# Kernel optimization log

Measured on AMD Instinct MI355X. Metric: run time of the kernel, lower is better.

Reference implementation:

```python
import jax, jax.numpy as jnp
import numpy as np

PHI = 0.1  # fraction of pruned weights randomized per inference


def setup_inputs() -> dict:
    key = jax.random.key(0)
    k1, k2, k3 = jax.random.split(key, 3)
    d_out, d_in, batch = 8192, 8192, 256
    W = jax.random.normal(k1, (d_out, d_in), jnp.float32) * 0.02
    prune = jax.random.uniform(k2, (d_out, d_in)) < 0.9
    W = jnp.where(prune, 0.0, W)
    mask = (W == 0.0)  # _register_masks: pruned positions
    x = jax.random.normal(k3, (batch, d_in), jnp.float32)
    return {"x": x, "W": W, "mask": mask}


def reference(x, W, mask):
    # --- _apply_random_flip (vectorized) ---
    n_pruned = int(np.asarray(jnp.sum(mask)))          # concrete mask -> static count
    n_flip = max(1, int(PHI * n_pruned))
    keep = ~mask
    n_keep = jnp.sum(keep).astype(W.dtype)
    wk = jnp.where(keep, W, 0.0)
    mean = jnp.sum(wk) / n_keep
    # torch .std() is unbiased (n-1 denominator)
    var = jnp.sum(jnp.where(keep, (W - mean) ** 2, 0.0)) / (n_keep - 1.0)
    std = jnp.sqrt(var)
    key = jax.random.key(42)
    ks, kv = jax.random.split(key)
    # uniform random permutation of pruned indices -> top_k of random scores
    scores = jnp.where(mask.ravel(), jax.random.uniform(ks, (W.size,)), -1.0)
    _, flip_idx = jax.lax.top_k(scores, n_flip)        # [n_flip] flat indices into W
    vals = jax.random.normal(kv, (n_flip,), W.dtype) * std * 0.1
    W_flipped = W.ravel().at[flip_idx].set(vals).reshape(W.shape)
    # --- base_model forward (Linear, no bias) ---
    out = x @ W_flipped.T                               # [batch, d_out]
    # --- _restore_masks: zero flipped weights again (no effect on out) ---
    _ = jnp.where(mask, 0.0, W_flipped)
    return out
```

## Files before the change

kernel.cpp:

```cpp
#include <hip/hip_runtime.h>

typedef unsigned int u32;
typedef unsigned long long u64;
typedef unsigned short u16;

#define NTOT   67108864u
#define T0P    7543296u
#define PBASE  14733u
#define NSUP   1651u
#define NWSEG  4096u
#define WCAP   2176u
#define RBLK   512u
#define SEGPB  8
#define RCAP   4352u
#define KSPLIT 4

struct Scalars {
  double sumW;
  double sumW2;
  u64 npruned;
  u64 nflip;
  float stdf;
  float pad;
};

#define OFF_COLSUM 0ull
#define OFF_SBASE  8192ull
#define OFF_SC     16384ull
#define OFF_SEGCNT 16512ull
#define OFF_XBF    33024ull
#define OFF_SEGS   4227328ull
#define OFF_ROUTED 39878912ull
#define OFF_WBF    75530496ull
#define WS_NEED_WBF 209748224ull
#define OFF_OUTP   OFF_SEGS

__host__ __device__ inline void tf2x32(u32 k0, u32 k1, u32 x0, u32 x1, u32& y0, u32& y1) {
  u32 ks2 = k0 ^ k1 ^ 0x1BD11BDAu;
  x0 += k0; x1 += k1;
#define TFR(r) { x0 += x1; x1 = (x1 << (r)) | (x1 >> (32 - (r))); x1 ^= x0; }
  TFR(13) TFR(15) TFR(26) TFR(6)  x0 += k1;  x1 += ks2 + 1u;
  TFR(17) TFR(29) TFR(16) TFR(24) x0 += ks2; x1 += k0 + 2u;
  TFR(13) TFR(15) TFR(26) TFR(6)  x0 += k0;  x1 += k1 + 3u;
  TFR(17) TFR(29) TFR(16) TFR(24) x0 += k1;  x1 += ks2 + 4u;
  TFR(13) TFR(15) TFR(26) TFR(6)  x0 += ks2; x1 += k0 + 5u;
#undef TFR
  y0 = x0; y1 = x1;
}

__device__ inline u32 jax_bits32(u32 k0, u32 k1, u32 i) {
  u32 y0, y1; tf2x32(k0, k1, 0u, i, y0, y1);
  return y0 ^ y1;
}

__device__ inline u16 f2bf(float f) {
  union { float f; u32 u; } c; c.f = f;
  u32 r = ((c.u >> 16) & 1u) + 0x7FFFu;
  return (u16)((c.u + r) >> 16);
}

__device__ inline float erfinv32(float x) {
  float w = -log1pf(-x * x);
  float p;
  if (w < 5.0f) {
    w -= 2.5f;
    p = 2.81022636e-08f;
    p = fmaf(p, w, 3.43273939e-07f);
    p = fmaf(p, w, -3.5233877e-06f);
    p = fmaf(p, w, -4.39150654e-06f);
    p = fmaf(p, w, 0.00021858087f);
    p = fmaf(p, w, -0.00125372503f);
    p = fmaf(p, w, -0.00417768164f);
    p = fmaf(p, w, 0.246640727f);
    p = fmaf(p, w, 1.50140941f);
  } else {
    w = sqrtf(w) - 3.0f;
    p = -0.000200214257f;
    p = fmaf(p, w, 0.000100950558f);
    p = fmaf(p, w, 0.00134934322f);
    p = fmaf(p, w, -0.00367342844f);
    p = fmaf(p, w, 0.00573950773f);
    p = fmaf(p, w, -0.0076224613f);
    p = fmaf(p, w, 0.00943887047f);
    p = fmaf(p, w, 1.00167406f);
    p = fmaf(p, w, 2.83297682f);
  }
  return p * x;
}

__global__ __launch_bounds__(256) void k_pass1w(const float* __restrict__ W,
                                                u16* __restrict__ wbf,
                                                const float* __restrict__ x,
                                                u16* __restrict__ xbf,
                                                Scalars* sc, u32* segcnt, u32* segs,
                                                u32 uk0, u32 uk1, u32 dowbf) {
  u32 t = threadIdx.x;
  u32 bid = blockIdx.x;
  if (bid < 1024u) {
    u32 gid = bid * 256 + t;
    u32 lane = t & 63;
    u32 wid = gid >> 6;
    u32* wseg = segs + (u64)wid * WCAP;
    u32 wbase = 0;
    float sf = 0.f, sf2 = 0.f; u32 cnt = 0;
    const u32 stride8 = 1024u * 256u * 8u;
    for (u32 b8 = gid * 8; b8 < NTOT; b8 += stride8) {
      float4 wa = *(const float4*)(W + b8);
      float4 wb = *(const float4*)(W + b8 + 4);
      u32 sb[8];
#pragma unroll
      for (int e = 0; e < 8; e++) sb[e] = jax_bits32(uk0, uk1, b8 + (u32)e) >> 9;
      float we[8] = {wa.x, wa.y, wa.z, wa.w, wb.x, wb.y, wb.z, wb.w};
      u32 cand[8]; u32 nc = 0;
#pragma unroll
      for (int e = 0; e < 8; e++) {
        float w = we[e];
        sf += w;
        sf2 = fmaf(w, w, sf2);
        bool pr = (w == 0.0f);
        cnt += pr ? 1u : 0u;
        if (pr && sb[e] >= T0P) { cand[nc] = b8 + (u32)e; nc++; }
      }
      u32 inc = nc;
#pragma unroll
      for (int o = 1; o < 64; o <<= 1) { u32 v = (u32)__shfl_up((int)inc, o); if (lane >= (u32)o) inc += v; }
      u32 tot = (u32)__shfl((int)inc, 63);
      u32 pos = wbase + inc - nc;
      for (u32 k2 = 0; k2 < nc; k2++)
        if (pos + k2 < WCAP) wseg[pos + k2] = cand[k2];
      wbase += tot;
    }
    double s = (double)sf, s2 = (double)sf2;
    for (int o = 32; o > 0; o >>= 1) {
      s += __shfl_down(s, o); s2 += __shfl_down(s2, o); cnt += __shfl_down(cnt, o);
    }
    if (lane == 0) {
      atomicAdd(&sc->sumW, s);
      atomicAdd(&sc->sumW2, s2);
      atomicAdd(&sc->npruned, (u64)cnt);
      segcnt[wid] = (wbase > WCAP) ? WCAP : wbase;
    }
  } else if (bid < 1984u) {
    if (!dowbf) return;
    u32 i0 = (bid - 1024u) * 256 + t;
    const u32 stride = 960u * 256u;
    for (u32 g = i0; g < NTOT / 8u; g += stride) {
      const float4* p = (const float4*)(W + (u64)g * 8);
      float4 a = p[0], b = p[1];
      uint4 o;
      o.x = (u32)f2bf(a.x) | ((u32)f2bf(a.y) << 16);
      o.y = (u32)f2bf(a.z) | ((u32)f2bf(a.w) << 16);
      o.z = (u32)f2bf(b.x) | ((u32)f2bf(b.y) << 16);
      o.w = (u32)f2bf(b.z) | ((u32)f2bf(b.w) << 16);
      *(uint4*)(wbf + (u64)g * 8) = o;
    }
  } else {
    u32 i0 = (bid - 1984u) * 256 + t;
    const u32 stride = 64u * 256u;
    for (u32 g = i0; g < 524288u; g += stride) {
      float4 v = ((const float4*)x)[g];
      ushort4 o; o.x = f2bf(v.x); o.y = f2bf(v.y); o.z = f2bf(v.z); o.w = f2bf(v.w);
      ((ushort4*)xbf)[g] = o;
    }
  }
}

__global__ __launch_bounds__(256) void k_route(const u32* __restrict__ segs,
                                               const u32* __restrict__ segcnt,
                                               u32* gcur, u32* routed,
                                               u32 uk0, u32 uk1) {
  __shared__ u32 lhist[2048];
  __shared__ u32 lbase[2048];
  u32 t = threadIdx.x;
  for (u32 j = t; j < 2048; j += 256) lhist[j] = 0;
  __syncthreads();
#pragma unroll 1
  for (int sg = 0; sg < SEGPB; sg++) {
    u32 wid = blockIdx.x * SEGPB + sg;
    u32 n = segcnt[wid]; if (n > WCAP) n = WCAP;
    const u32* sp = segs + (u64)wid * WCAP;
    for (u32 i = t; i < n; i += 256)
      atomicAdd(&lhist[(jax_bits32(uk0, uk1, sp[i]) >> 18) - PBASE], 1u);
  }
  __syncthreads();
  for (u32 j = t; j < 2048; j += 256) {
    u32 c = lhist[j];
    lbase[j] = c ? atomicAdd(&gcur[j], c) : 0u;
    lhist[j] = 0;
  }
  __syncthreads();
#pragma unroll 1
  for (int sg = 0; sg < SEGPB; sg++) {
    u32 wid = blockIdx.x * SEGPB + sg;
    u32 n = segcnt[wid]; if (n > WCAP) n = WCAP;
    const u32* sp = segs + (u64)wid * WCAP;
    for (u32 i = t; i < n; i += 256) {
      u32 idx = sp[i];
      u32 sup = (jax_bits32(uk0, uk1, idx) >> 18) - PBASE;
      u32 pos = lbase[sup] + atomicAdd(&lhist[sup], 1u);
      if (pos < RCAP) routed[(u64)sup * RCAP + pos] = idx;
    }
  }
}

__global__ __launch_bounds__(256) void k_scan(const u32* __restrict__ colsum, Scalars* sc,
                                              u32* sbase) {
  __shared__ u32 h[2048];
  __shared__ u32 wtmp[4];
  u32 t = threadIdx.x, lane = t & 63, wv = t >> 6;
  for (u32 j = t; j < 2048; j += 256) h[j] = colsum[j];
  __syncthreads();
  u32 a[8]; u32 s8 = 0;
#pragma unroll
  for (int k = 0; k < 8; k++) { a[k] = h[2047 - (t * 8 + k)]; s8 += a[k]; }
  u32 inc = s8;
#pragma unroll
  for (int o = 1; o < 64; o <<= 1) { u32 v = (u32)__shfl_up((int)inc, o); if (lane >= (u32)o) inc += v; }
  if (lane == 63) wtmp[wv] = inc;
  __syncthreads();
  u32 woff = 0; for (u32 w = 0; w < wv; w++) woff += wtmp[w];
  u32 base = woff + inc - s8;
#pragma unroll
  for (int k = 0; k < 8; k++) { sbase[2047 - (t * 8 + k)] = base; base += a[k]; }
  if (t == 0) {
    double nk = (double)NTOT - (double)sc->npruned;
    double mean = sc->sumW / nk;
    double var = (sc->sumW2 - 2.0 * mean * sc->sumW + nk * mean * mean) / (nk - 1.0);
    sc->stdf = (float)sqrt(var);
    u64 nfi = (u64)(0.1 * (double)sc->npruned);
    if (nfi < 1) nfi = 1;
    sc->nflip = nfi;
  }
}

__device__ inline void suf512(const u32* cnt, u32* suf, u32* wtmp) {
  u32 t = threadIdx.x, lane = t & 63, wv = t >> 6;
  u32 a0 = cnt[511 - t * 2], a1 = cnt[510 - t * 2];
  u32 s = a0 + a1;
  u32 inc = s;
#pragma unroll
  for (int o = 1; o < 64; o <<= 1) { u32 v = (u32)__shfl_up((int)inc, o); if (lane >= (u32)o) inc += v; }
  if (lane == 63) wtmp[wv] = inc;
  __syncthreads();
  u32 woff = 0;
  for (u32 w = 0; w < wv; w++) woff += wtmp[w];
  u32 base = woff + inc - s;
  suf[511 - t * 2] = base;
  suf[510 - t * 2] = base + a0;
  __syncthreads();
}

template<int MODE>
__global__ __launch_bounds__(256) void k_rank(float* __restrict__ W,
                                              u16* __restrict__ wbf,
                                              const u32* __restrict__ colsum,
                                              const u32* __restrict__ sbase,
                                              const u32* __restrict__ routed,
                                              const Scalars* __restrict__ sc,
                                              u32 uk0, u32 uk1, u32 vk0, u32 vk1) {
  u32 p = blockIdx.x;
  u32 n = colsum[p]; if (n == 0) return;
  if (n > RCAP) n = RCAP;
  u64 nflip = sc->nflip;
  u32 rbase = sbase[p];
  if ((u64)rbase >= nflip) return;
  __shared__ u16 sFine[RCAP];
  __shared__ u32 pIdx[RCAP];
  __shared__ u32 hist[512], gbase[512], cur[512], wtmp[4];
  u32 t = threadIdx.x;
  for (u32 j = t; j < 512; j += 256) hist[j] = 0;
  __syncthreads();
  const u32* src = routed + (u64)p * RCAP;
  for (u32 i = t; i < n; i += 256) {
    u32 f = (jax_bits32(uk0, uk1, src[i]) >> 9) & 511u;
    sFine[i] = (u16)f;
    atomicAdd(&hist[f], 1u);
  }
  __syncthreads();
  suf512(hist, gbase, wtmp);
  for (u32 j = t; j < 512; j += 256) cur[j] = gbase[j];
  __syncthreads();
  for (u32 i = t; i < n; i += 256) {
    u32 pos = atomicAdd(&cur[sFine[i]], 1u);
    pIdx[pos] = src[i];
  }
  __syncthreads();
  float stdf = sc->stdf;
  for (u32 i = t; i < n; i += 256) {
    u32 f = sFine[i];
    u32 g0 = gbase[f], g1 = g0 + hist[f];
    u32 v = src[i];
    u32 ord = 0;
    for (u32 q = g0; q < g1; q++) ord += (pIdx[q] < v) ? 1u : 0u;
    u64 rank = (u64)rbase + g0 + ord;
    if (rank >= nflip) continue;
    u32 bits = jax_bits32(vk0, vk1, (u32)rank);
    union { u32 u; float fl; } cv; cv.u = 0x3F800000u | (bits >> 9);
    float fu = cv.fl - 1.0f;
    const float lo = -0.99999994f;
    float u2 = fmaxf(lo, fu * 2.0f + lo);
    float nrm = 1.41421354f * erfinv32(u2);
    float val = (nrm * stdf) * 0.1f;
    if (MODE == 1) wbf[v] = f2bf(val);
    else           W[v] = val;
  }
}

typedef __bf16 bf16x8 __attribute__((ext_vector_type(8)));
typedef float f32x4 __attribute__((ext_vector_type(4)));

__global__ __launch_bounds__(256, 3) void k_gemm2(const u16* __restrict__ xbf,
                                                  const u16* __restrict__ wbf,
                                                  float* __restrict__ outp) {
  __shared__ u16 As[128 * 64];
  __shared__ u16 Bs[128 * 64];
  u32 i = blockIdx.x;
  u32 xcd = i & 7u, slot = i >> 3;
  u32 mi = slot & 1u, qq = slot >> 1;
  u32 pid = xcd * 32u + qq;
  u32 kidx = pid >> 6;
  u32 nb = pid & 63u;
  u32 mrow = mi * 128u, nrow = nb * 128u;
  u32 kbase = kidx * 2048u;
  u32 tid = threadIdx.x;
  u32 lane = tid & 63, wv = tid >> 6;
  u32 l8 = lane & 7;
  u32 lr = lane >> 3;
  u32 wm = wv >> 1, wn = wv & 1;
  u32 r = lane & 15, q = lane >> 4;
  f32x4 acc[4][4];
#pragma unroll
  for (int a = 0; a < 4; a++)
#pragma unroll
    for (int b = 0; b < 4; b++) acc[a][b] = (f32x4){0.f, 0.f, 0.f, 0.f};

  for (u32 kb = kbase; kb < kbase + 2048u; kb += 64u) {
#pragma unroll
    for (int j = 0; j < 4; j++) {
      u32 g = wv * 4 + (u32)j;
      u32 row = g * 8 + lr;
      u32 sc = ((l8 ^ (row & 7u)) * 8u);
      const u16* ga = xbf + (u64)(mrow + row) * 8192 + kb + sc;
      __builtin_amdgcn_global_load_lds((const u32*)ga, (u32*)&As[g * 512u], 16, 0, 0);
      const u16* gb = wbf + (u64)(nrow + row) * 8192 + kb + sc;
      __builtin_amdgcn_global_load_lds((const u32*)gb, (u32*)&Bs[g * 512u], 16, 0, 0);
    }
    __syncthreads();
#pragma unroll
    for (int ks = 0; ks < 2; ks++) {
      bf16x8 a[4], b[4];
      u32 ch = (u32)(ks * 4) + q;
#pragma unroll
      for (int mt = 0; mt < 4; mt++) {
        u32 row = wm * 64 + (u32)mt * 16 + r;
        a[mt] = *(bf16x8*)&As[row * 64 + ((ch ^ (r & 7u)) * 8u)];
      }
#pragma unroll
      for (int nt = 0; nt < 4; nt++) {
        u32 row = wn * 64 + (u32)nt * 16 + r;
        b[nt] = *(bf16x8*)&Bs[row * 64 + ((ch ^ (r & 7u)) * 8u)];
      }
#pragma unroll
      for (int mt = 0; mt < 4; mt++)
#pragma unroll
        for (int nt = 0; nt < 4; nt++)
          acc[mt][nt] = __builtin_amdgcn_mfma_f32_16x16x32_bf16(a[mt], b[nt], acc[mt][nt], 0, 0, 0);
    }
    __syncthreads();
  }
  float* op = outp + (u64)kidx * 2097152u;
  u32 quad = lane >> 4, col = lane & 15;
#pragma unroll
  for (int mt = 0; mt < 4; mt++)
#pragma unroll
    for (int nt = 0; nt < 4; nt++) {
      u32 n = nrow + wn * 64 + (u32)nt * 16 + col;
#pragma unroll
      for (int rg = 0; rg < 4; rg++) {
        u32 m = mrow + wm * 64 + (u32)mt * 16 + quad * 4 + (u32)rg;
        op[(u64)m * 8192 + n] = acc[mt][nt][rg];
      }
    }
}

__global__ __launch_bounds__(256) void k_redout(const float* __restrict__ part,
                                                float* __restrict__ out) {
  u32 i = blockIdx.x * 256 + threadIdx.x;
  float4 s = ((const float4*)part)[i];
#pragma unroll
  for (int k = 1; k < KSPLIT; k++) {
    float4 v = ((const float4*)(part + (u64)k * 2097152u))[i];
    s.x += v.x; s.y += v.y; s.z += v.z; s.w += v.w;
  }
  ((float4*)out)[i] = s;
}

__global__ __launch_bounds__(256, 2) void k_gemm_fb(const u16* __restrict__ xbf,
                                                    const float* __restrict__ W,
                                                    float* __restrict__ out) {
  __shared__ u16 xs[256 * 72];
  __shared__ u16 wsm[64 * 72];
  u32 tid = threadIdx.x;
  u32 lane = tid & 63, wv = tid >> 6;
  u32 nt0 = blockIdx.x * 64;
  u32 kbase = blockIdx.y * 2048u;
  f32x4 acc[4][4];
#pragma unroll
  for (int i = 0; i < 4; i++)
#pragma unroll
    for (int j = 0; j < 4; j++) acc[i][j] = (f32x4){0.f, 0.f, 0.f, 0.f};
  for (u32 kb = kbase; kb < kbase + 2048u; kb += 64u) {
#pragma unroll
    for (int r8 = 0; r8 < 8; r8++) {
      u32 row = r8 * 32 + (tid >> 3);
      u32 kseg = (tid & 7) * 8;
      uint4 v = *(const uint4*)(xbf + (u64)row * 8192 + kb + kseg);
      *(uint4*)&xs[row * 72 + kseg] = v;
    }
#pragma unroll
    for (int rr = 0; rr < 4; rr++) {
      u32 f4 = rr * 256 + tid;
      u32 row = f4 >> 4;
      u32 kc = (f4 & 15) * 4;
      float4 v = *(const float4*)(W + (u64)(nt0 + row) * 8192 + kb + kc);
      ushort4 o; o.x = f2bf(v.x); o.y = f2bf(v.y); o.z = f2bf(v.z); o.w = f2bf(v.w);
      *(ushort4*)&wsm[row * 72 + kc] = o;
    }
    __syncthreads();
#pragma unroll
    for (int ks = 0; ks < 2; ks++) {
      bf16x8 a[4], b[4];
      u32 koff = ks * 32 + (lane >> 4) * 8;
      u32 rsel = lane & 15;
#pragma unroll
      for (int mt = 0; mt < 4; mt++) a[mt] = *(bf16x8*)&xs[(wv * 64 + mt * 16 + rsel) * 72 + koff];
#pragma unroll
      for (int nt = 0; nt < 4; nt++) b[nt] = *(bf16x8*)&wsm[(nt * 16 + rsel) * 72 + koff];
#pragma unroll
      for (int mt = 0; mt < 4; mt++)
#pragma unroll
        for (int nt = 0; nt < 4; nt++)
          acc[mt][nt] = __builtin_amdgcn_mfma_f32_16x16x32_bf16(a[mt], b[nt], acc[mt][nt], 0, 0, 0);
    }
    __syncthreads();
  }
  u32 quad = lane >> 4, col = lane & 15;
#pragma unroll
  for (int mt = 0; mt < 4; mt++)
#pragma unroll
    for (int nt = 0; nt < 4; nt++) {
      u32 n = nt0 + nt * 16 + col;
#pragma unroll
      for (int rg = 0; rg < 4; rg++) {
        u32 m = wv * 64 + mt * 16 + quad * 4 + rg;
        atomicAdd(&out[(u64)m * 8192 + n], acc[mt][nt][rg]);
      }
    }
}

extern "C" void kernel_launch(void* const* d_in, const int* in_sizes, int n_in,
                              void* d_out, int out_size, void* d_ws, size_t ws_size,
                              hipStream_t stream) {
  const float* x; float* W;
  if (in_sizes[0] == 2097152) { x = (const float*)d_in[0]; W = (float*)d_in[1]; }
  else                        { x = (const float*)d_in[1]; W = (float*)d_in[0]; }
  float* out = (float*)d_out;
  char* ws = (char*)d_ws;

  u32* colsum = (u32*)(ws + OFF_COLSUM);
  u32* sbase  = (u32*)(ws + OFF_SBASE);
  Scalars* sc = (Scalars*)(ws + OFF_SC);
  u32* segcnt = (u32*)(ws + OFF_SEGCNT);
  u16* xbf    = (u16*)(ws + OFF_XBF);
  u32* segs   = (u32*)(ws + OFF_SEGS);
  u32* routed = (u32*)(ws + OFF_ROUTED);
  u16* wbf    = (u16*)(ws + OFF_WBF);
  float* outp = (float*)(ws + OFF_OUTP);

  bool t1 = (ws_size >= (size_t)WS_NEED_WBF);

  u32 a0, a1, b0, b1;
  tf2x32(0u, 42u, 0u, 0u, a0, a1);
  tf2x32(0u, 42u, 0u, 1u, b0, b1);

  hipMemsetAsync(sc, 0, sizeof(Scalars), stream);
  hipMemsetAsync(colsum, 0, 2048 * sizeof(u32), stream);

  u32 dowbf = t1 ? 1u : 0u;
  k_pass1w<<<2048, 256, 0, stream>>>(W, wbf, x, xbf, sc, segcnt, segs, a0, a1, dowbf);
  k_route<<<RBLK, 256, 0, stream>>>(segs, segcnt, colsum, routed, a0, a1);
  k_scan<<<1, 256, 0, stream>>>(colsum, sc, sbase);
  if (t1) {
    k_rank<1><<<NSUP, 256, 0, stream>>>(W, wbf, colsum, sbase, routed, sc, a0, a1, b0, b1);
    k_gemm2<<<512, 256, 0, stream>>>(xbf, wbf, outp);
    k_gemm2<<<512, 256, 0, stream>>>(xbf, wbf, outp);
    k_redout<<<2048, 256, 0, stream>>>(outp, out);
  } else {
    k_rank<0><<<NSUP, 256, 0, stream>>>(W, wbf, colsum, sbase, routed, sc, a0, a1, b0, b1);
    hipMemsetAsync(out, 0, (size_t)out_size * 4, stream);
    dim3 g(128, 4);
    k_gemm_fb<<<g, 256, 0, stream>>>(xbf, W, out);
  }
}
```

Measured before the change: 976.4 us.

## Patch flipped weights into GEMM LDS tiles instead of scattering into bf16 W

When the workspace is large enough, k_rank no longer scatters random values into the bf16 weight copy. It writes (index, value) pairs to a flat list instead. A new partition kernel buckets these pairs by (output block, k-tile), and the GEMM overwrites the matching LDS B-tile entries after each tile load. The aim is to replace millions of random 2-byte global writes with sequential writes plus LDS patches, at the cost of an extra kernel, a bucket buffer and an extra barrier per k-step. The duplicated k_gemm2 launch is also dropped in both bf16 paths.

```diff
diff --git a/kernel.cpp b/kernel.cpp
--- a/kernel.cpp
+++ b/kernel.cpp
@@ -14,6 +14,9 @@
 #define SEGPB  8
 #define RCAP   4352u
 #define KSPLIT 4
+#define FLIPCAP 6291456u
+#define NBKT2  8192u
+#define BCAP2  1144u
 
 struct Scalars {
   double sumW;
@@ -33,6 +36,10 @@
 #define OFF_ROUTED 39878912ull
 #define OFF_WBF    75530496ull
 #define WS_NEED_WBF 209748224ull
+#define OFF_FLIPF  209748224ull
+#define OFF_FB2    260079872ull
+#define OFF_BCUR2  335053056ull
+#define WS_NEED_T3 335085824ull
 #define OFF_OUTP   OFF_SEGS
 
 __host__ __device__ inline void tf2x32(u32 k0, u32 k1, u32 x0, u32 x1, u32& y0, u32& y1) {
@@ -253,6 +260,7 @@
 template<int MODE>
 __global__ __launch_bounds__(256) void k_rank(float* __restrict__ W,
                                               u16* __restrict__ wbf,
+                                              u64* __restrict__ flipflat,
                                               const u32* __restrict__ colsum,
                                               const u32* __restrict__ sbase,
                                               const u32* __restrict__ routed,
@@ -301,16 +309,57 @@
     float u2 = fmaxf(lo, fu * 2.0f + lo);
     float nrm = 1.41421354f * erfinv32(u2);
     float val = (nrm * stdf) * 0.1f;
-    if (MODE == 1) wbf[v] = f2bf(val);
-    else           W[v] = val;
+    if (MODE == 2) {
+      if (rank < (u64)FLIPCAP) flipflat[rank] = ((u64)v << 16) | (u64)f2bf(val);
+    } else if (MODE == 1) {
+      wbf[v] = f2bf(val);
+    } else {
+      W[v] = val;
+    }
+  }
+}
+
+__global__ __launch_bounds__(256) void k_part(const u64* __restrict__ flipflat,
+                                              const Scalars* __restrict__ sc,
+                                              u64* __restrict__ fb2,
+                                              u32* __restrict__ bcur2) {
+  __shared__ u32 lhist[NBKT2];
+  __shared__ u32 lbase[NBKT2];
+  u32 t = threadIdx.x;
+  u32 nf = (u32)sc->nflip; if (nf > FLIPCAP) nf = FLIPCAP;
+  u32 per = (nf + 511u) / 512u;
+  u32 lo = blockIdx.x * per;
+  u32 hi = lo + per; if (hi > nf) hi = nf;
+  for (u32 j = t; j < NBKT2; j += 256) lhist[j] = 0;
+  __syncthreads();
+  for (u32 i = lo + t; i < hi; i += 256) {
+    u32 v = (u32)(flipflat[i] >> 16) & 0x3FFFFFFu;
+    atomicAdd(&lhist[(v >> 20) * 128u + ((v >> 6) & 127u)], 1u);
+  }
+  __syncthreads();
+  for (u32 j = t; j < NBKT2; j += 256) {
+    u32 c = lhist[j];
+    lbase[j] = c ? atomicAdd(&bcur2[j], c) : 0u;
+    lhist[j] = 0;
+  }
+  __syncthreads();
+  for (u32 i = lo + t; i < hi; i += 256) {
+    u64 pk = flipflat[i];
+    u32 v = (u32)(pk >> 16) & 0x3FFFFFFu;
+    u32 b = (v >> 20) * 128u + ((v >> 6) & 127u);
+    u32 pos = lbase[b] + atomicAdd(&lhist[b], 1u);
+    if (pos < BCAP2) fb2[(u64)b * BCAP2 + pos] = pk;
   }
 }
 
 typedef __bf16 bf16x8 __attribute__((ext_vector_type(8)));
 typedef float f32x4 __attribute__((ext_vector_type(4)));
 
+template<int PATCH>
 __global__ __launch_bounds__(256, 3) void k_gemm2(const u16* __restrict__ xbf,
                                                   const u16* __restrict__ wbf,
+                                                  const u64* __restrict__ fb2,
+                                                  const u32* __restrict__ bcur2,
                                                   float* __restrict__ outp) {
   __shared__ u16 As[128 * 64];
   __shared__ u16 Bs[128 * 64];
@@ -346,6 +395,19 @@
       __builtin_amdgcn_global_load_lds((const u32*)gb, (u32*)&Bs[g * 512u], 16, 0, 0);
     }
     __syncthreads();
+    if (PATCH) {
+      u32 bkt = nb * 128u + (kb >> 6);
+      u32 pc = bcur2[bkt]; if (pc > BCAP2) pc = BCAP2;
+      const u64* fp = fb2 + (u64)bkt * BCAP2;
+      for (u32 ii = tid; ii < pc; ii += 256) {
+        u64 pk = fp[ii];
+        u32 v = (u32)(pk >> 16) & 0x3FFFFFFu;
+        u32 rr = (v >> 13) & 127u;
+        u32 cc = v & 63u;
+        Bs[rr * 64u + (((cc >> 3) ^ (rr & 7u)) << 3) + (cc & 7u)] = (u16)pk;
+      }
+      __syncthreads();
+    }
 #pragma unroll
     for (int ks = 0; ks < 2; ks++) {
       bf16x8 a[4], b[4];
@@ -476,7 +538,11 @@
   u32* routed = (u32*)(ws + OFF_ROUTED);
   u16* wbf    = (u16*)(ws + OFF_WBF);
   float* outp = (float*)(ws + OFF_OUTP);
-
+  u64* flipflat = (u64*)(ws + OFF_FLIPF);
+  u64* fb2      = (u64*)(ws + OFF_FB2);
+  u32* bcur2    = (u32*)(ws + OFF_BCUR2);
+
+  bool t3 = (ws_size >= (size_t)WS_NEED_T3);
   bool t1 = (ws_size >= (size_t)WS_NEED_WBF);
 
   u32 a0, a1, b0, b1;
@@ -485,18 +551,23 @@
 
   hipMemsetAsync(sc, 0, sizeof(Scalars), stream);
   hipMemsetAsync(colsum, 0, 2048 * sizeof(u32), stream);
+  if (t3) hipMemsetAsync(bcur2, 0, NBKT2 * sizeof(u32), stream);
 
   u32 dowbf = t1 ? 1u : 0u;
   k_pass1w<<<2048, 256, 0, stream>>>(W, wbf, x, xbf, sc, segcnt, segs, a0, a1, dowbf);
   k_route<<<RBLK, 256, 0, stream>>>(segs, segcnt, colsum, routed, a0, a1);
   k_scan<<<1, 256, 0, stream>>>(colsum, sc, sbase);
-  if (t1) {
-    k_rank<1><<<NSUP, 256, 0, stream>>>(W, wbf, colsum, sbase, routed, sc, a0, a1, b0, b1);
-    k_gemm2<<<512, 256, 0, stream>>>(xbf, wbf, outp);
-    k_gemm2<<<512, 256, 0, stream>>>(xbf, wbf, outp);
+  if (t3) {
+    k_rank<2><<<NSUP, 256, 0, stream>>>(W, wbf, flipflat, colsum, sbase, routed, sc, a0, a1, b0, b1);
+    k_part<<<512, 256, 0, stream>>>(flipflat, sc, fb2, bcur2);
+    k_gemm2<1><<<512, 256, 0, stream>>>(xbf, wbf, fb2, bcur2, outp);
+    k_redout<<<2048, 256, 0, stream>>>(outp, out);
+  } else if (t1) {
+    k_rank<1><<<NSUP, 256, 0, stream>>>(W, wbf, flipflat, colsum, sbase, routed, sc, a0, a1, b0, b1);
+    k_gemm2<0><<<512, 256, 0, stream>>>(xbf, wbf, fb2, bcur2, outp);
     k_redout<<<2048, 256, 0, stream>>>(outp, out);
   } else {
-    k_rank<0><<<NSUP, 256, 0, stream>>>(W, wbf, colsum, sbase, routed, sc, a0, a1, b0, b1);
+    k_rank<0><<<NSUP, 256, 0, stream>>>(W, wbf, flipflat, colsum, sbase, routed, sc, a0, a1, b0, b1);
     hipMemsetAsync(out, 0, (size_t)out_size * 4, stream);
     dim3 g(128, 4);
     k_gemm_fb<<<g, 256, 0, stream>>>(xbf, W, out);
```

Measured after the change: 1.071 ms. 1.1x slower.

## Carry random bits with candidate indices and drop the duplicate GEMM launch

Applied to the files above, without the earlier changes.

The first pass now stores each candidate as a 64-bit word holding its threefry random bits next to its flat index. The route and rank kernels read those bits back instead of rerunning jax_bits32 on every candidate. The second, redundant k_gemm2 launch is also removed. In exchange, the segment and routed buffers double in size and the routed buffer moves, which raises the workspace needed for the bf16 path and may push smaller workspaces onto the slower fallback.

```diff
diff --git a/kernel.cpp b/kernel.cpp
--- a/kernel.cpp
+++ b/kernel.cpp
@@ -8,6 +8,7 @@
 #define T0P    7543296u
 #define PBASE  14733u
 #define NSUP   1651u
+#define P1BLK  1024u
 #define NWSEG  4096u
 #define WCAP   2176u
 #define RBLK   512u
@@ -30,9 +31,11 @@
 #define OFF_SEGCNT 16512ull
 #define OFF_XBF    33024ull
 #define OFF_SEGS   4227328ull
-#define OFF_ROUTED 39878912ull
 #define OFF_WBF    75530496ull
-#define WS_NEED_WBF 209748224ull
+#define OFF_ROUTED 209748224ull
+#define WS_NEED_T1 281051392ull
+#define OFF_ROUTED_FB OFF_WBF
+#define WS_NEED_FB 146833664ull
 #define OFF_OUTP   OFF_SEGS
 
 __host__ __device__ inline void tf2x32(u32 k0, u32 k1, u32 x0, u32 x1, u32& y0, u32& y1) {
@@ -92,18 +95,18 @@
                                                 u16* __restrict__ wbf,
                                                 const float* __restrict__ x,
                                                 u16* __restrict__ xbf,
-                                                Scalars* sc, u32* segcnt, u32* segs,
+                                                Scalars* sc, u32* segcnt, u64* segs,
                                                 u32 uk0, u32 uk1, u32 dowbf) {
   u32 t = threadIdx.x;
   u32 bid = blockIdx.x;
-  if (bid < 1024u) {
+  if (bid < P1BLK) {
     u32 gid = bid * 256 + t;
     u32 lane = t & 63;
     u32 wid = gid >> 6;
-    u32* wseg = segs + (u64)wid * WCAP;
+    u64* wseg = segs + (u64)wid * WCAP;
     u32 wbase = 0;
     float sf = 0.f, sf2 = 0.f; u32 cnt = 0;
-    const u32 stride8 = 1024u * 256u * 8u;
+    const u32 stride8 = P1BLK * 256u * 8u;
     for (u32 b8 = gid * 8; b8 < NTOT; b8 += stride8) {
       float4 wa = *(const float4*)(W + b8);
       float4 wb = *(const float4*)(W + b8 + 4);
@@ -111,7 +114,7 @@
 #pragma unroll
       for (int e = 0; e < 8; e++) sb[e] = jax_bits32(uk0, uk1, b8 + (u32)e) >> 9;
       float we[8] = {wa.x, wa.y, wa.z, wa.w, wb.x, wb.y, wb.z, wb.w};
-      u32 cand[8]; u32 nc = 0;
+      u64 cand[8]; u32 nc = 0;
 #pragma unroll
       for (int e = 0; e < 8; e++) {
         float w = we[e];
@@ -119,7 +122,7 @@
         sf2 = fmaf(w, w, sf2);
         bool pr = (w == 0.0f);
         cnt += pr ? 1u : 0u;
-        if (pr && sb[e] >= T0P) { cand[nc] = b8 + (u32)e; nc++; }
+        if (pr && sb[e] >= T0P) { cand[nc] = ((u64)sb[e] << 32) | (u64)(b8 + (u32)e); nc++; }
       }
       u32 inc = nc;
 #pragma unroll
@@ -142,7 +145,7 @@
     }
   } else if (bid < 1984u) {
     if (!dowbf) return;
-    u32 i0 = (bid - 1024u) * 256 + t;
+    u32 i0 = (bid - P1BLK) * 256 + t;
     const u32 stride = 960u * 256u;
     for (u32 g = i0; g < NTOT / 8u; g += stride) {
       const float4* p = (const float4*)(W + (u64)g * 8);
@@ -165,10 +168,9 @@
   }
 }
 
-__global__ __launch_bounds__(256) void k_route(const u32* __restrict__ segs,
+__global__ __launch_bounds__(256) void k_route(const u64* __restrict__ segs,
                                                const u32* __restrict__ segcnt,
-                                               u32* gcur, u32* routed,
-                                               u32 uk0, u32 uk1) {
+                                               u32* gcur, u64* routed) {
   __shared__ u32 lhist[2048];
   __shared__ u32 lbase[2048];
   u32 t = threadIdx.x;
@@ -178,9 +180,9 @@
   for (int sg = 0; sg < SEGPB; sg++) {
     u32 wid = blockIdx.x * SEGPB + sg;
     u32 n = segcnt[wid]; if (n > WCAP) n = WCAP;
-    const u32* sp = segs + (u64)wid * WCAP;
+    const u64* sp = segs + (u64)wid * WCAP;
     for (u32 i = t; i < n; i += 256)
-      atomicAdd(&lhist[(jax_bits32(uk0, uk1, sp[i]) >> 18) - PBASE], 1u);
+      atomicAdd(&lhist[(u32)(sp[i] >> 41) - PBASE], 1u);
   }
   __syncthreads();
   for (u32 j = t; j < 2048; j += 256) {
@@ -193,12 +195,12 @@
   for (int sg = 0; sg < SEGPB; sg++) {
     u32 wid = blockIdx.x * SEGPB + sg;
     u32 n = segcnt[wid]; if (n > WCAP) n = WCAP;
-    const u32* sp = segs + (u64)wid * WCAP;
+    const u64* sp = segs + (u64)wid * WCAP;
     for (u32 i = t; i < n; i += 256) {
-      u32 idx = sp[i];
-      u32 sup = (jax_bits32(uk0, uk1, idx) >> 18) - PBASE;
+      u64 pk = sp[i];
+      u32 sup = (u32)(pk >> 41) - PBASE;
       u32 pos = lbase[sup] + atomicAdd(&lhist[sup], 1u);
-      if (pos < RCAP) routed[(u64)sup * RCAP + pos] = idx;
+      if (pos < RCAP) routed[(u64)sup * RCAP + pos] = pk;
     }
   }
 }
@@ -255,9 +257,9 @@
                                               u16* __restrict__ wbf,
                                               const u32* __restrict__ colsum,
                                               const u32* __restrict__ sbase,
-                                              const u32* __restrict__ routed,
+                                              const u64* __restrict__ routed,
                                               const Scalars* __restrict__ sc,
-                                              u32 uk0, u32 uk1, u32 vk0, u32 vk1) {
+                                              u32 vk0, u32 vk1) {
   u32 p = blockIdx.x;
   u32 n = colsum[p]; if (n == 0) return;
   if (n > RCAP) n = RCAP;
@@ -270,9 +272,9 @@
   u32 t = threadIdx.x;
   for (u32 j = t; j < 512; j += 256) hist[j] = 0;
   __syncthreads();
-  const u32* src = routed + (u64)p * RCAP;
+  const u64* src = routed + (u64)p * RCAP;
   for (u32 i = t; i < n; i += 256) {
-    u32 f = (jax_bits32(uk0, uk1, src[i]) >> 9) & 511u;
+    u32 f = (u32)(src[i] >> 32) & 511u;
     sFine[i] = (u16)f;
     atomicAdd(&hist[f], 1u);
   }
@@ -282,14 +284,14 @@
   __syncthreads();
   for (u32 i = t; i < n; i += 256) {
     u32 pos = atomicAdd(&cur[sFine[i]], 1u);
-    pIdx[pos] = src[i];
+    pIdx[pos] = (u32)src[i];
   }
   __syncthreads();
   float stdf = sc->stdf;
   for (u32 i = t; i < n; i += 256) {
     u32 f = sFine[i];
     u32 g0 = gbase[f], g1 = g0 + hist[f];
-    u32 v = src[i];
+    u32 v = (u32)src[i];
     u32 ord = 0;
     for (u32 q = g0; q < g1; q++) ord += (pIdx[q] < v) ? 1u : 0u;
     u64 rank = (u64)rbase + g0 + ord;
@@ -472,12 +474,12 @@
   Scalars* sc = (Scalars*)(ws + OFF_SC);
   u32* segcnt = (u32*)(ws + OFF_SEGCNT);
   u16* xbf    = (u16*)(ws + OFF_XBF);
-  u32* segs   = (u32*)(ws + OFF_SEGS);
-  u32* routed = (u32*)(ws + OFF_ROUTED);
+  u64* segs   = (u64*)(ws + OFF_SEGS);
   u16* wbf    = (u16*)(ws + OFF_WBF);
   float* outp = (float*)(ws + OFF_OUTP);
 
-  bool t1 = (ws_size >= (size_t)WS_NEED_WBF);
+  bool t1 = (ws_size >= (size_t)WS_NEED_T1);
+  u64* routed = t1 ? (u64*)(ws + OFF_ROUTED) : (u64*)(ws + OFF_ROUTED_FB);
 
   u32 a0, a1, b0, b1;
   tf2x32(0u, 42u, 0u, 0u, a0, a1);
@@ -488,15 +490,14 @@
 
   u32 dowbf = t1 ? 1u : 0u;
   k_pass1w<<<2048, 256, 0, stream>>>(W, wbf, x, xbf, sc, segcnt, segs, a0, a1, dowbf);
-  k_route<<<RBLK, 256, 0, stream>>>(segs, segcnt, colsum, routed, a0, a1);
+  k_route<<<RBLK, 256, 0, stream>>>(segs, segcnt, colsum, routed);
   k_scan<<<1, 256, 0, stream>>>(colsum, sc, sbase);
   if (t1) {
-    k_rank<1><<<NSUP, 256, 0, stream>>>(W, wbf, colsum, sbase, routed, sc, a0, a1, b0, b1);
-    k_gemm2<<<512, 256, 0, stream>>>(xbf, wbf, outp);
+    k_rank<1><<<NSUP, 256, 0, stream>>>(W, wbf, colsum, sbase, routed, sc, b0, b1);
     k_gemm2<<<512, 256, 0, stream>>>(xbf, wbf, outp);
     k_redout<<<2048, 256, 0, stream>>>(outp, out);
   } else {
-    k_rank<0><<<NSUP, 256, 0, stream>>>(W, wbf, colsum, sbase, routed, sc, a0, a1, b0, b1);
+    k_rank<0><<<NSUP, 256, 0, stream>>>(W, wbf, colsum, sbase, routed, sc, b0, b1);
     hipMemsetAsync(out, 0, (size_t)out_size * 4, stream);
     dim3 g(128, 4);
     k_gemm_fb<<<g, 256, 0, stream>>>(xbf, W, out);
```

After: 950.8 us. -2.6%, faster.
